# Optimization experiments

Hardware: AMD Instinct MI355X
Metric: run time of the kernel (lower is better)

The kernel has to match this reference:

```python
import jax, jax.numpy as jnp
import numpy as np

D_MODEL = 1024
NUM_HEADS = 16
D_K = D_MODEL // NUM_HEADS


def setup_inputs() -> dict:
    key = jax.random.key(0)
    ks = jax.random.split(key, 12)
    B, S = 2, 2048
    s = 1.0 / np.sqrt(D_MODEL)
    inp = {
        'q': jax.random.normal(ks[0], (B, S, D_MODEL), jnp.float32),
        'k': jax.random.normal(ks[1], (B, S, D_MODEL), jnp.float32),
        'v': jax.random.normal(ks[2], (B, S, D_MODEL), jnp.float32),
        'mask': jax.random.randint(ks[3], (B, S, S), 0, 2, jnp.int32),
        'Wq_w': jax.random.normal(ks[4], (D_MODEL, D_MODEL), jnp.float32) * s,
        'Wq_b': jnp.zeros((D_MODEL,), jnp.float32),
        'Wk_w': jax.random.normal(ks[5], (D_MODEL, D_MODEL), jnp.float32) * s,
        'Wk_b': jnp.zeros((D_MODEL,), jnp.float32),
        'Wv_w': jax.random.normal(ks[6], (D_MODEL, D_MODEL), jnp.float32) * s,
        'Wv_b': jnp.zeros((D_MODEL,), jnp.float32),
        'Wo_w': jax.random.normal(ks[7], (D_MODEL, D_MODEL), jnp.float32) * s,
        'Wo_b': jnp.zeros((D_MODEL,), jnp.float32),
    }
    return inp


def reference(q, k, v, mask, Wq_w, Wq_b, Wk_w, Wk_b, Wv_w, Wv_b, Wo_w, Wo_b):
    B, Sq, _ = q.shape
    # torch Linear: x @ W.T + b
    qp = (q @ Wq_w.T + Wq_b).reshape(B, Sq, NUM_HEADS, D_K)
    kp = (k @ Wk_w.T + Wk_b).reshape(B, k.shape[1], NUM_HEADS, D_K)
    vp = (v @ Wv_w.T + Wv_b).reshape(B, v.shape[1], NUM_HEADS, D_K)
    # scores: [B, H, Sq, Sk]
    scores = jnp.einsum('bqhd,bkhd->bhqk', qp, kp) / np.sqrt(D_K).astype(np.float32)
    scores = jnp.where(mask[:, None, :, :] == 0, jnp.float32(-10000.0), scores)
    attn = jax.nn.softmax(scores, axis=-1)
    ctx = jnp.einsum('bhqk,bkhd->bqhd', attn, vp).reshape(B, Sq, D_MODEL)
    return ctx @ Wo_w.T + Wo_b
```

## Files before the change

### kernel.cpp

```cpp
#include <hip/hip_runtime.h>

#define DM   1024
#define HN   16
#define DKH  64
#define SEQ  2048
#define BATCH 2

typedef __attribute__((ext_vector_type(8))) __bf16 bf16x8;
typedef __attribute__((ext_vector_type(4))) float  f32x4;

#define AS1 __attribute__((address_space(1)))
#define AS3 __attribute__((address_space(3)))
#define GLL(g, l) __builtin_amdgcn_global_load_lds((const AS1 unsigned int*)(const void*)(g), \
                                                   (AS3 unsigned int*)(void*)(l), 16, 0, 0)

__device__ __forceinline__ unsigned short f2bf(float f) {
  union { float f; unsigned u; } v; v.f = f;
  unsigned u = v.u;
  u += 0x7FFFu + ((u >> 16) & 1u);
  return (unsigned short)(u >> 16);
}

__global__ __launch_bounds__(256) void prep_kernel(
    const float* __restrict__ q, const float* __restrict__ k,
    const float* __restrict__ v,
    const float* __restrict__ Wq, const float* __restrict__ Wk,
    const float* __restrict__ Wv, const float* __restrict__ Wo,
    const int* __restrict__ mask,
    unsigned short* __restrict__ q_bf, unsigned short* __restrict__ k_bf,
    unsigned short* __restrict__ v_bf,
    unsigned short* __restrict__ Wq_bf, unsigned short* __restrict__ Wk_bf,
    unsigned short* __restrict__ Wv_bf, unsigned short* __restrict__ Wo_bf,
    unsigned* __restrict__ pkm) {
  const int bid = blockIdx.x;
  if (bid < 12288) {
    int t = bid >> 12, r = bid & 4095;
    const float* in = (t == 0) ? q : (t == 1) ? k : v;
    unsigned short* out = (t == 0) ? q_bf : (t == 1) ? k_bf : v_bf;
    int i = r * 256 + threadIdx.x;
    float4 f = ((const float4*)in)[i];
    ushort4 o;
    o.x = f2bf(f.x); o.y = f2bf(f.y); o.z = f2bf(f.z); o.w = f2bf(f.w);
    ((ushort4*)out)[i] = o;
  } else if (bid < 16384) {
    int b2 = bid - 12288;
    int t = b2 >> 10, r = b2 & 1023;
    const float* in = (t == 0) ? Wq : (t == 1) ? Wk : (t == 2) ? Wv : Wo;
    unsigned short* out = (t == 0) ? Wq_bf : (t == 1) ? Wk_bf : (t == 2) ? Wv_bf : Wo_bf;
    int i = r * 256 + threadIdx.x;
    float4 f = ((const float4*)in)[i];
    ushort4 o;
    o.x = f2bf(f.x); o.y = f2bf(f.y); o.z = f2bf(f.z); o.w = f2bf(f.w);
    ((ushort4*)out)[i] = o;
  } else {
    int W = (bid - 16384) * 256 + threadIdx.x;
    const int4* base = (const int4*)(mask + (size_t)(W >> 6) * SEQ + (size_t)(W & 63) * 32);
    unsigned bits = 0;
#pragma unroll
    for (int g = 0; g < 8; ++g) {
      int4 m = base[g];
      bits |= (unsigned)(m.x != 0) << (4 * g);
      bits |= (unsigned)(m.y != 0) << (4 * g + 1);
      bits |= (unsigned)(m.z != 0) << (4 * g + 2);
      bits |= (unsigned)(m.w != 0) << (4 * g + 3);
    }
    pkm[W] = bits;
  }
}

__device__ __forceinline__ void gemm_core_pipe(
    const unsigned short* __restrict__ A,
    const unsigned short* __restrict__ W,
    unsigned short* lds,
    f32x4 (&acc)[4][4]) {
  const int tid = threadIdx.x;
  const int wave = tid >> 6, lane = tid & 63;
  const int l15 = lane & 15, quad = lane >> 4;
  const int wr = wave >> 1, wc = wave & 1;

  const int rl = lane >> 2;
  const int cg = (lane & 3) ^ (((rl & 3) + ((rl >> 2) & 3)) & 3);
  const unsigned short* ga = A + (size_t)(wave * 32 + rl) * DM + cg * 8;
  const unsigned short* gb = W + (size_t)(wave * 32 + rl) * DM + cg * 8;
  unsigned short* la = lds + wave * 1024;
  unsigned short* lb = lds + 4096 + wave * 1024;

  const int cfr = (quad ^ (((l15 & 3) + ((l15 >> 2) & 3)) & 3)) * 8;

  auto stage = [&](int ki, int sb) {
    const unsigned short* a = ga + ki * 32;
    const unsigned short* b = gb + ki * 32;
    GLL(a, la + sb);                    GLL(a + (size_t)16 * DM, la + sb + 512);
    GLL(b, lb + sb);                    GLL(b + (size_t)16 * DM, lb + sb + 512);
  };
  auto compute = [&](int sb) {
    const unsigned short* Ab = lds + sb;
    const unsigned short* Bb = lds + sb + 4096;
    bf16x8 af[4], bfr[4];
#pragma unroll
    for (int mt = 0; mt < 4; ++mt)
      af[mt] = *(const bf16x8*)(Ab + (size_t)(wr * 64 + mt * 16 + l15) * 32 + cfr);
#pragma unroll
    for (int nt = 0; nt < 4; ++nt)
      bfr[nt] = *(const bf16x8*)(Bb + (size_t)(wc * 64 + nt * 16 + l15) * 32 + cfr);
#pragma unroll
    for (int mt = 0; mt < 4; ++mt)
#pragma unroll
      for (int nt = 0; nt < 4; ++nt)
        acc[mt][nt] = __builtin_amdgcn_mfma_f32_16x16x32_bf16(af[mt], bfr[nt], acc[mt][nt], 0, 0, 0);
  };

  stage(0, 0);
  stage(1, 8192);
  int sb0 = 0, sb1 = 8192, sb2 = 16384;
#pragma unroll 1
  for (int i = 0; i < DM / 32 - 2; ++i) {
    stage(i + 2, sb2);
    asm volatile("s_waitcnt vmcnt(8)\ns_barrier" ::: "memory");
    compute(sb0);
    asm volatile("s_barrier" ::: "memory");
    int t = sb0; sb0 = sb1; sb1 = sb2; sb2 = t;
  }
  asm volatile("s_waitcnt vmcnt(4)\ns_barrier" ::: "memory");
  compute(sb0);
  asm volatile("s_waitcnt vmcnt(0)\ns_barrier" ::: "memory");
  compute(sb1);
}

__global__ __launch_bounds__(256, 3) void gemm_qkv(
    const unsigned short* __restrict__ Aq, const unsigned short* __restrict__ Ak,
    const unsigned short* __restrict__ Av,
    const unsigned short* __restrict__ Wq, const unsigned short* __restrict__ Wk,
    const unsigned short* __restrict__ Wv,
    const float* __restrict__ bq, const float* __restrict__ bk,
    const float* __restrict__ bv,
    unsigned short* __restrict__ oq, unsigned short* __restrict__ ok,
    unsigned short* __restrict__ ovT) {
  const int z = blockIdx.z;
  const unsigned short* A = (z == 0) ? Aq : (z == 1) ? Ak : Av;
  const unsigned short* W = (z == 0) ? Wq : (z == 1) ? Wk : Wv;
  const float* bias = (z == 0) ? bq : (z == 1) ? bk : bv;

  __shared__ __align__(16) unsigned short lds[24576];

  const int bn = blockIdx.x * 128, bm = blockIdx.y * 128;
  f32x4 acc[4][4] = {};
  gemm_core_pipe(A + (size_t)bm * DM, W + (size_t)bn * DM, lds, acc);

  const int tid = threadIdx.x;
  const int wave = tid >> 6, lane = tid & 63;
  const int l15 = lane & 15, quad = lane >> 4;
  const int wr = wave >> 1, wc = wave & 1;

  if (z != 2) {
    const float qs = (z == 0) ? 0.125f * 1.44269504088896f : 1.0f;
    unsigned short* out = (z == 0) ? oq : ok;
#pragma unroll
    for (int mt = 0; mt < 4; ++mt)
#pragma unroll
      for (int nt = 0; nt < 4; ++nt) {
        int col = bn + wc * 64 + nt * 16 + l15;
        float bb = bias[col];
#pragma unroll
        for (int r = 0; r < 4; ++r) {
          int row = bm + wr * 64 + mt * 16 + quad * 4 + r;
          out[(size_t)row * DM + col] = f2bf((acc[mt][nt][r] + bb) * qs);
        }
      }
  } else {
    unsigned short* LT = lds;
    __syncthreads();
#pragma unroll
    for (int mt = 0; mt < 4; ++mt)
#pragma unroll
      for (int nt = 0; nt < 4; ++nt) {
        int c = wc * 64 + nt * 16 + l15;
        float bb = bias[bn + c];
        int t0 = wr * 64 + mt * 16 + quad * 4;
        ushort4 w4;
        w4.x = f2bf(acc[mt][nt][0] + bb);
        w4.y = f2bf(acc[mt][nt][1] + bb);
        w4.z = f2bf(acc[mt][nt][2] + bb);
        w4.w = f2bf(acc[mt][nt][3] + bb);
        *(ushort4*)(LT + (size_t)c * 136 + t0) = w4;
      }
    __syncthreads();
    const int b = bm >> 11, sbase = bm & (SEQ - 1);
#pragma unroll
    for (int j = 0; j < 8; ++j) {
      int c = wave * 32 + (j >> 1) * 8 + (lane >> 3);
      int tk = (j & 1) * 64 + (lane & 7) * 8;
      bf16x8 vv = *(const bf16x8*)(LT + (size_t)c * 136 + tk);
      int C = bn + c;
      int h = C >> 6, dk = C & 63;
      *(bf16x8*)(ovT + ((size_t)((b * HN + h) * DKH + dk)) * SEQ + sbase + tk) = vv;
    }
  }
}

__global__ __launch_bounds__(256, 3) void gemm_wo(
    const unsigned short* __restrict__ A, const unsigned short* __restrict__ W,
    const float* __restrict__ bias, float* __restrict__ out) {
  __shared__ __align__(16) unsigned short lds[24576];

  const int bn = blockIdx.x * 128, bm = blockIdx.y * 128;
  f32x4 acc[4][4] = {};
  gemm_core_pipe(A + (size_t)bm * DM, W + (size_t)bn * DM, lds, acc);

  const int tid = threadIdx.x;
  const int wave = tid >> 6, lane = tid & 63;
  const int l15 = lane & 15, quad = lane >> 4;
  const int wr = wave >> 1, wc = wave & 1;

#pragma unroll
  for (int mt = 0; mt < 4; ++mt)
#pragma unroll
    for (int nt = 0; nt < 4; ++nt) {
      int col = bn + wc * 64 + nt * 16 + l15;
      float bb = bias[col];
#pragma unroll
      for (int r = 0; r < 4; ++r) {
        int row = bm + wr * 64 + mt * 16 + quad * 4 + r;
        out[(size_t)row * DM + col] = acc[mt][nt][r] + bb;
      }
    }
}

__global__ __launch_bounds__(256, 4) void attn_kernel(
    const unsigned short* __restrict__ qp,
    const unsigned short* __restrict__ kp,
    const unsigned short* __restrict__ vpT,
    const unsigned* __restrict__ pk,
    unsigned short* __restrict__ ctx) {
  const int lane = threadIdx.x & 63;
  const int wave = threadIdx.x >> 6;
  const int l15 = lane & 15, quad = lane >> 4;
  const int bh = blockIdx.x;
  const int b = bh >> 4, h = bh & 15;
  const int qrow = blockIdx.y * 64 + wave * 16 + l15;

  __shared__ __align__(16) unsigned short lds[16384];

  const unsigned short* qb = qp + ((size_t)(b * SEQ + qrow)) * DM + h * DKH + quad * 8;
  bf16x8 qf0 = *(const bf16x8*)qb;
  bf16x8 qf1 = *(const bf16x8*)(qb + 32);

  f32x4 o[4] = {};
  f32x4 lacc = {};
  bf16x8 ones;
#pragma unroll
  for (int i = 0; i < 8; ++i) ones[i] = (__bf16)1.0f;

  const int i8 = lane >> 3;
  const int cs = lane & 7;
  const int cg0 = cs ^ i8;
  const int cg1 = cs ^ i8 ^ 4;
  const unsigned short* kg0 = kp + ((size_t)(b * SEQ + wave * 16 + i8)) * DM + h * DKH + cg0 * 8;
  const unsigned short* kg1 = kp + ((size_t)(b * SEQ + wave * 16 + 8 + i8)) * DM + h * DKH + cg1 * 8;
  const unsigned short* vg0 = vpT + ((size_t)(bh * DKH + wave * 16 + i8)) * SEQ + cg0 * 8;
  const unsigned short* vg1 = vpT + ((size_t)(bh * DKH + wave * 16 + 8 + i8)) * SEQ + cg1 * 8;
  unsigned short* lK = lds + wave * 1024;
  unsigned short* lV = lds + 8192 + wave * 1024;

  const int perm = ((l15 >> 2) << 3) | (l15 & 3);
  int kofs[2][2];
#pragma unroll
  for (int s = 0; s < 2; ++s)
#pragma unroll
    for (int u = 0; u < 2; ++u) {
      int r = perm + 4 * u + 32 * s;
      int sw = (r & 7) ^ (((r >> 3) & 1) << 2);
      kofs[s][u] = r * 64 + ((quad ^ sw) * 8);
    }
  int vofs[4];
#pragma unroll
  for (int t = 0; t < 4; ++t) {
    int r = t * 16 + l15;
    int sw = (r & 7) ^ (((r >> 3) & 1) << 2);
    vofs[t] = r * 64 + ((quad ^ sw) * 8);
  }

  const unsigned* mb = pk + (size_t)(b * SEQ + qrow) * (SEQ / 32);

  auto compute_tile = [&](int j0, const unsigned short* Kb, const unsigned short* Vb) {
    uint2 mw = *(const uint2*)(mb + (j0 >> 5));
    unsigned bx = mw.x >> (quad * 8);
    unsigned by = mw.y >> (quad * 8);

    f32x4 sc[2][2];
#pragma unroll
    for (int s = 0; s < 2; ++s)
#pragma unroll
      for (int u = 0; u < 2; ++u) {
        bf16x8 k0 = *(const bf16x8*)(Kb + kofs[s][u]);
        bf16x8 k1 = *(const bf16x8*)(Kb + (kofs[s][u] ^ 32));
        f32x4 a = {};
        a = __builtin_amdgcn_mfma_f32_16x16x32_bf16(k0, qf0, a, 0, 0, 0);
        a = __builtin_amdgcn_mfma_f32_16x16x32_bf16(k1, qf1, a, 0, 0, 0);
        sc[s][u] = a;
      }

    float p[2][2][4];
#pragma unroll
    for (int s = 0; s < 2; ++s)
#pragma unroll
      for (int u = 0; u < 2; ++u) {
        unsigned bits = s ? by : bx;
#pragma unroll
        for (int r = 0; r < 4; ++r) {
          float e = __builtin_amdgcn_exp2f(sc[s][u][r]);
          p[s][u][r] = ((bits >> (4 * u + r)) & 1u) ? e : 0.0f;
        }
      }

    bf16x8 pb[2];
#pragma unroll
    for (int s = 0; s < 2; ++s) {
      bf16x8 t;
      t[0] = (__bf16)p[s][0][0]; t[1] = (__bf16)p[s][0][1];
      t[2] = (__bf16)p[s][0][2]; t[3] = (__bf16)p[s][0][3];
      t[4] = (__bf16)p[s][1][0]; t[5] = (__bf16)p[s][1][1];
      t[6] = (__bf16)p[s][1][2]; t[7] = (__bf16)p[s][1][3];
      pb[s] = t;
    }

#pragma unroll
    for (int s = 0; s < 2; ++s) {
      lacc = __builtin_amdgcn_mfma_f32_16x16x32_bf16(ones, pb[s], lacc, 0, 0, 0);
#pragma unroll
      for (int t = 0; t < 4; ++t) {
        bf16x8 vf = *(const bf16x8*)(Vb + (vofs[t] ^ (s ? 32 : 0)));
        o[t] = __builtin_amdgcn_mfma_f32_16x16x32_bf16(vf, pb[s], o[t], 0, 0, 0);
      }
    }
  };

  GLL(kg0, lK);           GLL(kg1, lK + 512);
  GLL(vg0, lV);           GLL(vg1, lV + 512);

#pragma unroll 1
  for (int j0 = 0; j0 < SEQ; j0 += 128) {
    __syncthreads();
    if (j0 + 64 < SEQ) {
      GLL(kg0 + (size_t)(j0 + 64) * DM, lK + 4096);
      GLL(kg1 + (size_t)(j0 + 64) * DM, lK + 4096 + 512);
      GLL(vg0 + (j0 + 64), lV + 4096);
      GLL(vg1 + (j0 + 64), lV + 4096 + 512);
    }
    compute_tile(j0, lds, lds + 8192);

    __syncthreads();
    if (j0 + 128 < SEQ) {
      GLL(kg0 + (size_t)(j0 + 128) * DM, lK);
      GLL(kg1 + (size_t)(j0 + 128) * DM, lK + 512);
      GLL(vg0 + (j0 + 128), lV);
      GLL(vg1 + (j0 + 128), lV + 512);
    }
    compute_tile(j0 + 64, lds + 4096, lds + 12288);
  }

  float inv = 1.0f / lacc[0];
#pragma unroll
  for (int t = 0; t < 4; ++t) {
    ushort4 w;
    w.x = f2bf(o[t][0] * inv);
    w.y = f2bf(o[t][1] * inv);
    w.z = f2bf(o[t][2] * inv);
    w.w = f2bf(o[t][3] * inv);
    *(ushort4*)(ctx + ((size_t)(b * SEQ + qrow)) * DM + h * DKH + t * 16 + quad * 4) = w;
  }
}

extern "C" void kernel_launch(void* const* d_in, const int* in_sizes, int n_in,
                              void* d_out, int out_size, void* d_ws, size_t ws_size,
                              hipStream_t stream) {
  const float* q    = (const float*)d_in[0];
  const float* k    = (const float*)d_in[1];
  const float* v    = (const float*)d_in[2];
  const int*   mask = (const int*)d_in[3];
  const float* Wq_w = (const float*)d_in[4];
  const float* Wq_b = (const float*)d_in[5];
  const float* Wk_w = (const float*)d_in[6];
  const float* Wk_b = (const float*)d_in[7];
  const float* Wv_w = (const float*)d_in[8];
  const float* Wv_b = (const float*)d_in[9];
  const float* Wo_w = (const float*)d_in[10];
  const float* Wo_b = (const float*)d_in[11];

  char* ws = (char*)d_ws;
  const size_t MB = 1024 * 1024;
  unsigned short* q_bf  = (unsigned short*)(ws + 0 * MB);
  unsigned short* k_bf  = (unsigned short*)(ws + 8 * MB);
  unsigned short* v_bf  = (unsigned short*)(ws + 16 * MB);
  unsigned short* Wq_bf = (unsigned short*)(ws + 24 * MB);
  unsigned short* Wk_bf = (unsigned short*)(ws + 26 * MB);
  unsigned short* Wv_bf = (unsigned short*)(ws + 28 * MB);
  unsigned short* Wo_bf = (unsigned short*)(ws + 30 * MB);
  unsigned short* qp    = (unsigned short*)(ws + 32 * MB);
  unsigned short* kp    = (unsigned short*)(ws + 40 * MB);
  unsigned short* vpT   = (unsigned short*)(ws + 48 * MB);
  unsigned short* ctx   = (unsigned short*)(ws + 56 * MB);
  unsigned* pkm = (unsigned*)d_out;

  const int M = BATCH * SEQ;

  prep_kernel<<<17408, 256, 0, stream>>>(q, k, v, Wq_w, Wk_w, Wv_w, Wo_w, mask,
                                         q_bf, k_bf, v_bf, Wq_bf, Wk_bf, Wv_bf,
                                         Wo_bf, pkm);

  gemm_qkv<<<dim3(DM / 128, M / 128, 3), 256, 0, stream>>>(
      q_bf, k_bf, v_bf, Wq_bf, Wk_bf, Wv_bf, Wq_b, Wk_b, Wv_b, qp, kp, vpT);

  attn_kernel<<<dim3(BATCH * HN, SEQ / 64), 256, 0, stream>>>(qp, kp, vpT, pkm, ctx);

  gemm_wo<<<dim3(DM / 128, M / 128), 256, 0, stream>>>(ctx, Wo_bf, Wo_b, (float*)d_out);
}
```

Measured before the change: 138.4 us.

## Switch attention to 32x32x16 MFMA with 128-row query tiles per block

Rewrites the attention inner loop to use 32x32x16 bf16 MFMA instructions, so each wave handles 32 query rows and each block 128 rows. This halves the number of blocks and the K/V LDS traffic per query row. Score-to-probability packing now uses v_cvt_pk_bf16_f32 and permlane32_swap to rearrange the MFMA output layout into operand layout. The change raises register pressure, lowers launch bounds occupancy to 2, and the output stores become scattered 2-byte writes.

```diff
diff --git a/kernel.cpp b/kernel.cpp
--- a/kernel.cpp
+++ b/kernel.cpp
@@ -8,6 +8,8 @@
 
 typedef __attribute__((ext_vector_type(8))) __bf16 bf16x8;
 typedef __attribute__((ext_vector_type(4))) float  f32x4;
+typedef __attribute__((ext_vector_type(16))) float f32x16;
+typedef __attribute__((ext_vector_type(2)))  int   i32x2;
 
 #define AS1 __attribute__((address_space(1)))
 #define AS3 __attribute__((address_space(3)))
@@ -226,7 +228,7 @@
     }
 }
 
-__global__ __launch_bounds__(256, 4) void attn_kernel(
+__global__ __launch_bounds__(256, 2) void attn_kernel(
     const unsigned short* __restrict__ qp,
     const unsigned short* __restrict__ kp,
     const unsigned short* __restrict__ vpT,
@@ -234,104 +236,97 @@
     unsigned short* __restrict__ ctx) {
   const int lane = threadIdx.x & 63;
   const int wave = threadIdx.x >> 6;
-  const int l15 = lane & 15, quad = lane >> 4;
+  const int l31 = lane & 31, hi = lane >> 5, l7 = lane & 7;
   const int bh = blockIdx.x;
   const int b = bh >> 4, h = bh & 15;
-  const int qrow = blockIdx.y * 64 + wave * 16 + l15;
+  const int qrow = blockIdx.y * 128 + wave * 32 + l31;
 
   __shared__ __align__(16) unsigned short lds[16384];
 
-  const unsigned short* qb = qp + ((size_t)(b * SEQ + qrow)) * DM + h * DKH + quad * 8;
-  bf16x8 qf0 = *(const bf16x8*)qb;
-  bf16x8 qf1 = *(const bf16x8*)(qb + 32);
-
-  f32x4 o[4] = {};
-  f32x4 lacc = {};
+  const unsigned short* qb = qp + ((size_t)(b * SEQ + qrow)) * DM + h * DKH + hi * 8;
+  bf16x8 qf[4];
+#pragma unroll
+  for (int kt = 0; kt < 4; ++kt) qf[kt] = *(const bf16x8*)(qb + kt * 16);
+
+  f32x16 o0 = {}, o1 = {}, lacc = {};
   bf16x8 ones;
 #pragma unroll
   for (int i = 0; i < 8; ++i) ones[i] = (__bf16)1.0f;
 
-  const int i8 = lane >> 3;
-  const int cs = lane & 7;
-  const int cg0 = cs ^ i8;
-  const int cg1 = cs ^ i8 ^ 4;
-  const unsigned short* kg0 = kp + ((size_t)(b * SEQ + wave * 16 + i8)) * DM + h * DKH + cg0 * 8;
-  const unsigned short* kg1 = kp + ((size_t)(b * SEQ + wave * 16 + 8 + i8)) * DM + h * DKH + cg1 * 8;
-  const unsigned short* vg0 = vpT + ((size_t)(bh * DKH + wave * 16 + i8)) * SEQ + cg0 * 8;
-  const unsigned short* vg1 = vpT + ((size_t)(bh * DKH + wave * 16 + 8 + i8)) * SEQ + cg1 * 8;
+  const int r8 = lane >> 3;
+  const int cg = (l7 ^ r8) * 8;
+  const unsigned short* kg0 = kp + ((size_t)(b * SEQ + wave * 16 + r8)) * DM + h * DKH + cg;
+  const unsigned short* kg1 = kg0 + (size_t)8 * DM;
+  const unsigned short* vg0 = vpT + ((size_t)(bh * DKH + wave * 16 + r8)) * SEQ + cg;
+  const unsigned short* vg1 = vg0 + (size_t)8 * SEQ;
   unsigned short* lK = lds + wave * 1024;
   unsigned short* lV = lds + 8192 + wave * 1024;
 
-  const int perm = ((l15 >> 2) << 3) | (l15 & 3);
-  int kofs[2][2];
-#pragma unroll
-  for (int s = 0; s < 2; ++s)
-#pragma unroll
-    for (int u = 0; u < 2; ++u) {
-      int r = perm + 4 * u + 32 * s;
-      int sw = (r & 7) ^ (((r >> 3) & 1) << 2);
-      kofs[s][u] = r * 64 + ((quad ^ sw) * 8);
-    }
-  int vofs[4];
-#pragma unroll
-  for (int t = 0; t < 4; ++t) {
-    int r = t * 16 + l15;
-    int sw = (r & 7) ^ (((r >> 3) & 1) << 2);
-    vofs[t] = r * 64 + ((quad ^ sw) * 8);
-  }
+  int roff[4];
+#pragma unroll
+  for (int x = 0; x < 4; ++x)
+    roff[x] = l31 * 64 + (((x * 2 + hi) ^ l7) * 8);
 
   const unsigned* mb = pk + (size_t)(b * SEQ + qrow) * (SEQ / 32);
+
+  auto make_pa = [&](const f32x16& sc, unsigned bits, bf16x8& paA, bf16x8& paB) {
+    float p[16];
+#pragma unroll
+    for (int r = 0; r < 16; ++r) {
+      float e = __builtin_amdgcn_exp2f(sc[r]);
+      p[r] = ((bits >> ((r & 3) + 8 * (r >> 2))) & 1u) ? e : 0.0f;
+    }
+    unsigned X0, X1, Y0, Y1;
+    asm("v_cvt_pk_bf16_f32 %0, %1, %2" : "=v"(X0) : "v"(p[0]), "v"(p[1]));
+    asm("v_cvt_pk_bf16_f32 %0, %1, %2" : "=v"(X1) : "v"(p[2]), "v"(p[3]));
+    asm("v_cvt_pk_bf16_f32 %0, %1, %2" : "=v"(Y0) : "v"(p[4]), "v"(p[5]));
+    asm("v_cvt_pk_bf16_f32 %0, %1, %2" : "=v"(Y1) : "v"(p[6]), "v"(p[7]));
+    i32x2 s0 = __builtin_amdgcn_permlane32_swap((int)X0, (int)Y0, false, false);
+    i32x2 s1 = __builtin_amdgcn_permlane32_swap((int)X1, (int)Y1, false, false);
+    union { unsigned u[4]; bf16x8 v; } ua;
+    ua.u[0] = (unsigned)s0.x; ua.u[1] = (unsigned)s1.x;
+    ua.u[2] = (unsigned)s0.y; ua.u[3] = (unsigned)s1.y;
+    paA = ua.v;
+    asm("v_cvt_pk_bf16_f32 %0, %1, %2" : "=v"(X0) : "v"(p[8]),  "v"(p[9]));
+    asm("v_cvt_pk_bf16_f32 %0, %1, %2" : "=v"(X1) : "v"(p[10]), "v"(p[11]));
+    asm("v_cvt_pk_bf16_f32 %0, %1, %2" : "=v"(Y0) : "v"(p[12]), "v"(p[13]));
+    asm("v_cvt_pk_bf16_f32 %0, %1, %2" : "=v"(Y1) : "v"(p[14]), "v"(p[15]));
+    s0 = __builtin_amdgcn_permlane32_swap((int)X0, (int)Y0, false, false);
+    s1 = __builtin_amdgcn_permlane32_swap((int)X1, (int)Y1, false, false);
+    union { unsigned u[4]; bf16x8 v; } ub;
+    ub.u[0] = (unsigned)s0.x; ub.u[1] = (unsigned)s1.x;
+    ub.u[2] = (unsigned)s0.y; ub.u[3] = (unsigned)s1.y;
+    paB = ub.v;
+  };
 
   auto compute_tile = [&](int j0, const unsigned short* Kb, const unsigned short* Vb) {
     uint2 mw = *(const uint2*)(mb + (j0 >> 5));
-    unsigned bx = mw.x >> (quad * 8);
-    unsigned by = mw.y >> (quad * 8);
-
-    f32x4 sc[2][2];
-#pragma unroll
-    for (int s = 0; s < 2; ++s)
-#pragma unroll
-      for (int u = 0; u < 2; ++u) {
-        bf16x8 k0 = *(const bf16x8*)(Kb + kofs[s][u]);
-        bf16x8 k1 = *(const bf16x8*)(Kb + (kofs[s][u] ^ 32));
-        f32x4 a = {};
-        a = __builtin_amdgcn_mfma_f32_16x16x32_bf16(k0, qf0, a, 0, 0, 0);
-        a = __builtin_amdgcn_mfma_f32_16x16x32_bf16(k1, qf1, a, 0, 0, 0);
-        sc[s][u] = a;
-      }
-
-    float p[2][2][4];
-#pragma unroll
-    for (int s = 0; s < 2; ++s)
-#pragma unroll
-      for (int u = 0; u < 2; ++u) {
-        unsigned bits = s ? by : bx;
-#pragma unroll
-        for (int r = 0; r < 4; ++r) {
-          float e = __builtin_amdgcn_exp2f(sc[s][u][r]);
-          p[s][u][r] = ((bits >> (4 * u + r)) & 1u) ? e : 0.0f;
-        }
-      }
-
-    bf16x8 pb[2];
-#pragma unroll
-    for (int s = 0; s < 2; ++s) {
-      bf16x8 t;
-      t[0] = (__bf16)p[s][0][0]; t[1] = (__bf16)p[s][0][1];
-      t[2] = (__bf16)p[s][0][2]; t[3] = (__bf16)p[s][0][3];
-      t[4] = (__bf16)p[s][1][0]; t[5] = (__bf16)p[s][1][1];
-      t[6] = (__bf16)p[s][1][2]; t[7] = (__bf16)p[s][1][3];
-      pb[s] = t;
-    }
-
-#pragma unroll
-    for (int s = 0; s < 2; ++s) {
-      lacc = __builtin_amdgcn_mfma_f32_16x16x32_bf16(ones, pb[s], lacc, 0, 0, 0);
-#pragma unroll
-      for (int t = 0; t < 4; ++t) {
-        bf16x8 vf = *(const bf16x8*)(Vb + (vofs[t] ^ (s ? 32 : 0)));
-        o[t] = __builtin_amdgcn_mfma_f32_16x16x32_bf16(vf, pb[s], o[t], 0, 0, 0);
-      }
+    unsigned bx = mw.x >> (4 * hi);
+    unsigned by = mw.y >> (4 * hi);
+
+    f32x16 sc0 = {}, sc1 = {};
+#pragma unroll
+    for (int kt = 0; kt < 4; ++kt) {
+      bf16x8 k0 = *(const bf16x8*)(Kb + roff[kt]);
+      bf16x8 k1 = *(const bf16x8*)(Kb + 2048 + roff[kt]);
+      sc0 = __builtin_amdgcn_mfma_f32_32x32x16_bf16(k0, qf[kt], sc0, 0, 0, 0);
+      sc1 = __builtin_amdgcn_mfma_f32_32x32x16_bf16(k1, qf[kt], sc1, 0, 0, 0);
+    }
+
+    bf16x8 pa[4];
+    make_pa(sc0, bx, pa[0], pa[1]);
+    make_pa(sc1, by, pa[2], pa[3]);
+
+#pragma unroll
+    for (int kc = 0; kc < 4; ++kc)
+      lacc = __builtin_amdgcn_mfma_f32_32x32x16_bf16(pa[kc], ones, lacc, 0, 0, 0);
+
+#pragma unroll
+    for (int kc = 0; kc < 4; ++kc) {
+      bf16x8 v0 = *(const bf16x8*)(Vb + roff[kc]);
+      bf16x8 v1 = *(const bf16x8*)(Vb + 2048 + roff[kc]);
+      o0 = __builtin_amdgcn_mfma_f32_32x32x16_bf16(pa[kc], v0, o0, 0, 0, 0);
+      o1 = __builtin_amdgcn_mfma_f32_32x32x16_bf16(pa[kc], v1, o1, 0, 0, 0);
     }
   };
 
@@ -359,15 +354,14 @@
     compute_tile(j0 + 64, lds + 4096, lds + 12288);
   }
 
-  float inv = 1.0f / lacc[0];
-#pragma unroll
-  for (int t = 0; t < 4; ++t) {
-    ushort4 w;
-    w.x = f2bf(o[t][0] * inv);
-    w.y = f2bf(o[t][1] * inv);
-    w.z = f2bf(o[t][2] * inv);
-    w.w = f2bf(o[t][3] * inv);
-    *(ushort4*)(ctx + ((size_t)(b * SEQ + qrow)) * DM + h * DKH + t * 16 + quad * 4) = w;
+  const int qbase = blockIdx.y * 128 + wave * 32;
+#pragma unroll
+  for (int r = 0; r < 16; ++r) {
+    int qg = qbase + (r & 3) + 8 * (r >> 2) + 4 * hi;
+    float inv = 1.0f / lacc[r];
+    unsigned short* op = ctx + ((size_t)(b * SEQ + qg)) * DM + h * DKH + l31;
+    op[0]  = f2bf(o0[r] * inv);
+    op[32] = f2bf(o1[r] * inv);
   }
 }
 
@@ -411,7 +405,7 @@
   gemm_qkv<<<dim3(DM / 128, M / 128, 3), 256, 0, stream>>>(
       q_bf, k_bf, v_bf, Wq_bf, Wk_bf, Wv_bf, Wq_b, Wk_b, Wv_b, qp, kp, vpT);
 
-  attn_kernel<<<dim3(BATCH * HN, SEQ / 64), 256, 0, stream>>>(qp, kp, vpT, pkm, ctx);
+  attn_kernel<<<dim3(BATCH * HN, SEQ / 128), 256, 0, stream>>>(qp, kp, vpT, pkm, ctx);
 
   gemm_wo<<<dim3(DM / 128, M / 128), 256, 0, stream>>>(ctx, Wo_bf, Wo_b, (float*)d_out);
 }
```

Result: faster. 134.4 us (-2.9%).
